# Performance work log

Measured on AMD Instinct MI355X. Metric: run time of the kernel, lower is better.

Reference implementation:

```python
import jax, jax.numpy as jnp
import numpy as np

B, F, S, K = 4, 1024, 2048, 7


def _activate_norm(x):
    # relu -> mean-center over last dim -> L2-normalize scaled by sqrt(n)
    out = jax.nn.relu(x)
    out = out - jnp.mean(out, axis=-1, keepdims=True)
    n = out.shape[-1]
    denom = (jnp.sqrt(jnp.sum(out * out, axis=-1, keepdims=True)) + 1e-5) * (n ** -0.5)
    return out / denom


def _causal_conv(x, w, k):
    # x: [B, C_in, S], w: [C_out, C_in, k]; left-pad by k-1 for causality
    return jax.lax.conv_general_dilated(
        x, w, window_strides=(1,), padding=[(k - 1, 0)],
        dimension_numbers=('NCH', 'OIH', 'NCH'))


def _feed_forward(x, w0, w1, k):
    return _causal_conv(_activate_norm(_causal_conv(x, w0, k)), w1, k)


def setup_inputs() -> dict:
    key = jax.random.key(0)
    ks = jax.random.split(key, 8)
    scale = 0.02
    inp = jax.random.normal(ks[0], (B, F, S), dtype=jnp.float32)
    pos_embd = jax.random.normal(ks[1], (1, F, S), dtype=jnp.float32) * scale
    divisor = jnp.arange(1, F + 1, dtype=jnp.float32).reshape(1, F, 1)
    ws = [jax.random.normal(ks[2 + i], (F, F, K), dtype=jnp.float32) * scale
          for i in range(6)]
    return {
        'inp': inp, 'pos_embd': pos_embd, 'divisor': divisor,
        'depth_w0': ws[0], 'depth_w1': ws[1],
        'point_w0': ws[2], 'point_w1': ws[3],
        'shift_w0': ws[4], 'shift_w1': ws[5],
    }


def reference(inp, pos_embd, divisor, depth_w0, depth_w1, point_w0, point_w1, shift_w0, shift_w1):
    out = inp + pos_embd
    depth = _feed_forward(out, depth_w0, depth_w1, K)
    point = _feed_forward(out, point_w0, point_w1, K)
    shift = _feed_forward(out, shift_w0, shift_w1, K)
    # linear attention: cumsum over feature axis (dim 1), matching depth.cumsum(1)
    return _activate_norm(inp * (jnp.cumsum(depth, axis=1) / divisor + point) + shift)
```

## Files before the change

### kernel.cpp

```cpp
#include <hip/hip_runtime.h>
#include <hip/hip_bf16.h>
#include <stdint.h>

#define B_ 4
#define F_ 1024
#define S_ 2048
#define K_ 7
#define SP_ (S_ + K_ - 1)
#define FC_ 64
#define NC_ (F_ / FC_)
#define FF_ ((size_t)F_ * F_)
#define BFS_ ((size_t)B_ * F_ * S_)
#define BSPF_ ((size_t)B_ * SP_ * F_)

using f32x4 = __attribute__((ext_vector_type(4))) float;
using s16x8 = __attribute__((ext_vector_type(8))) short;
using bf16 = __hip_bfloat16;

typedef const __attribute__((address_space(1))) void gvoid_t;
typedef __attribute__((address_space(3))) void lvoid_t;
__device__ __forceinline__ void async16(const void* g, void* l) {
    __builtin_amdgcn_global_load_lds((gvoid_t*)g, (lvoid_t*)l, 16, 0, 0);
}

__device__ __forceinline__ float bf2f(unsigned short u) {
    union { unsigned int i; float f; } c; c.i = ((unsigned int)u) << 16; return c.f;
}

#define FENCE() asm volatile("" ::: "memory")
#define BARRIER() do { FENCE(); __builtin_amdgcn_s_barrier(); FENCE(); } while (0)

__global__ void zero_pads(bf16* xT, bf16* hT, int nh) {
    int i = blockIdx.x * 256 + threadIdx.x;
    const int per = B_ * (K_ - 1) * F_;
    int total = (1 + nh) * per;
    if (i >= total) return;
    int r = i / per, o = i % per;
    int b = o / ((K_ - 1) * F_);
    int rr = o % ((K_ - 1) * F_);
    bf16 z = __float2bfloat16(0.0f);
    if (r == 0) xT[(size_t)b * SP_ * F_ + rr] = z;
    else        hT[(size_t)(r - 1) * BSPF_ + (size_t)b * SP_ * F_ + rr] = z;
}

__global__ void prep_x(const float* __restrict__ inp, const float* __restrict__ pos,
                       bf16* __restrict__ xT) {
    __shared__ bf16 tile[64][66];
    int b = blockIdx.z;
    int f0 = blockIdx.y * 64, s0 = blockIdx.x * 64;
    int tj = threadIdx.x & 63;
    int t4 = threadIdx.x >> 6;
#pragma unroll
    for (int r = 0; r < 16; ++r) {
        int i = r * 4 + t4;
        size_t off = (size_t)(f0 + i) * S_ + s0 + tj;
        float v = inp[(size_t)b * F_ * S_ + off] + pos[off];
        tile[i][tj] = __float2bfloat16(v);
    }
    __syncthreads();
#pragma unroll
    for (int r = 0; r < 16; ++r) {
        int j = r * 4 + t4;
        xT[(size_t)b * SP_ * F_ + (size_t)(6 + s0 + j) * F_ + f0 + tj] = tile[tj][j];
    }
}

__global__ void wconv(const float* __restrict__ w, bf16* __restrict__ wt) {
    int i = blockIdx.x * 256 + threadIdx.x;
    if (i >= F_ * F_) return;
    const float* src = w + (size_t)i * K_;
#pragma unroll
    for (int t = 0; t < K_; ++t)
        wt[(size_t)t * FF_ + i] = __float2bfloat16(src[t]);
}

#define MFMA_QUAD(MB, NB)                                                        \
    __builtin_amdgcn_s_setprio(1);                                               \
    _Pragma("unroll")                                                            \
    for (int kk = 0; kk < 2; ++kk) {                                             \
        _Pragma("unroll")                                                        \
        for (int m = 0; m < 4; ++m) {                                            \
            _Pragma("unroll")                                                    \
            for (int n = 0; n < 2; ++n) {                                        \
                acc[(MB) + m][(NB) + n] = __builtin_amdgcn_mfma_f32_16x16x32_bf16( \
                    af[m][kk], bfr[(NB) + n][kk], acc[(MB) + m][(NB) + n], 0, 0, 0); \
            }                                                                    \
        }                                                                        \
    }                                                                            \
    __builtin_amdgcn_s_setprio(0)

template <bool SPLIT>
__global__ __launch_bounds__(512, 2)
void conv_gemm8(const bf16* __restrict__ Wbase, const bf16* __restrict__ Xbase,
                bf16* __restrict__ O0, bf16* __restrict__ O1,
                long wStride, long xStride, long oStride) {
    __shared__ __align__(16) char lds[147456];

    int wg = blockIdx.x;
    int nchunk = gridDim.x >> 3;
    int swz = (wg & 7) * nchunk + (wg >> 3);
    int kp, r;
    if (SPLIT) { kp = swz & 1; r = swz >> 1; } else { kp = 0; r = swz; }
    int nt = r & 7;
    int mt = (r >> 3) & 3;
    int z  = r >> 5;
    int j = z >> 2, b = z & 3;
    const int kb0 = kp * 8;
    const int kbN = SPLIT ? 8 : 16;
    const int NTp = kbN * 7;

    const bf16* Wbr = Wbase + (size_t)j * wStride;
    const bf16* Xbr = Xbase + (size_t)j * xStride + (size_t)b * SP_ * F_;
    bf16* out = (kp ? O1 : O0) + (size_t)j * oStride + (size_t)b * F_ * S_;
    const int m0 = mt * 256, n0 = nt * 256;

    const int tid = threadIdx.x;
    const int lane = tid & 63, wid = tid >> 6;
    const int wm = wid >> 2, wn = wid & 3;

    const int tid16 = tid * 16;
    const int p0 = tid16, p1 = 8192 + tid16;
    const int lp0 = p0 ^ (((p0 >> 9) & 1) << 5);
    const int lp1 = p1 ^ (((p1 >> 9) & 1) << 5);
    const int stgO0 = (((lp0 >> 11) << 4) + ((lp0 >> 6) & 15)) * F_
                    + (((lp0 >> 10) & 1) << 5) + ((lp0 & 63) >> 1);
    const int stgO1 = (((lp1 >> 11) << 4) + ((lp1 >> 6) & 15)) * F_
                    + (((lp1 >> 10) & 1) << 5) + ((lp1 & 63) >> 1);
    const int bsrc = (((tid16 >> 11) << 4) + ((lp0 >> 6) & 15)) * F_
                   + (((lp0 >> 10) & 1) << 5) + ((lp0 & 63) >> 1);

    const int rA = lane & 15, cA = (lane >> 4) * 8;
    const int swzRC = (rA << 6) + ((cA << 1) ^ (((rA >> 3) & 1) << 5));
    const int aOffBase = wm * 16384 + swzRC;
    int addrB[7];
#pragma unroll
    for (int t = 0; t < 7; ++t) {
        int R = wn * 64 + rA + t;
        addrB[t] = ((R >> 4) << 11) + ((R & 15) << 6)
                 + ((cA << 1) ^ (((R >> 3) & 1) << 5));
    }

    f32x4 acc[8][4] = {};
    s16x8 af[4][2], bfr[4][2];

    auto STGA = [&](int regionByte, const bf16* src) {
        async16(src + stgO0, lds + regionByte + tid16);
        async16(src + stgO1, lds + regionByte + 8192 + tid16);
    };
    auto STGB = [&](int kb1, int pc) {
        const bf16* src = Xbr + (size_t)n0 * F_ + kb1 * 64 + bsrc + pc * 64 * F_;
        async16(src, lds + 65536 + (kb1 & 1) * 40960 + pc * 8192 + tid16);
    };
    auto ASRC = [&](int kb, int t, int h) {
        return Wbr + (size_t)t * FF_ + (size_t)(m0 + h * 128) * F_ + kb * 64;
    };

    STGB(kb0, 0); STGB(kb0, 1); STGB(kb0, 2); STGB(kb0, 3); STGB(kb0, 4);
    STGA(0,     ASRC(kb0, 0, 0));
    STGA(16384, ASRC(kb0, 0, 1));
    STGA(32768, ASRC(kb0, 1, 0));
    asm volatile("s_waitcnt vmcnt(2)" ::: "memory");
    BARRIER();

    for (int kb = kb0; kb < kb0 + kbN; ++kb) {
        const int bB = 65536 + (kb & 1) * 40960;
#pragma unroll
        for (int t = 0; t < 7; ++t) {
            const int ktl = (kb - kb0) * 7 + t;
            const int pA = (kb + t) & 1;
            const char* la = lds + pA * 32768 + aOffBase;
            const char* lb = lds + bB + addrB[t];
            const int t1 = (t == 6) ? 0 : t + 1;
            const int kb1 = (t == 6) ? kb + 1 : kb;
            const int t2 = (t >= 5) ? t - 5 : t + 2;
            const int kb2 = (t >= 5) ? kb + 1 : kb;
            const bool bstage = (t >= 1 && t <= 5) && (kb - kb0) < kbN - 1;

#pragma unroll
            for (int m = 0; m < 4; ++m) {
                af[m][0] = *(const s16x8*)(la + m * 2048);
                af[m][1] = *(const s16x8*)(la + m * 2048 + 1024);
            }
#pragma unroll
            for (int n = 0; n < 2; ++n) {
                bfr[n][0] = *(const s16x8*)(lb + n * 2048);
                bfr[n][1] = *(const s16x8*)(lb + n * 2048 + 1024);
            }
            if (ktl + 1 < NTp) STGA((pA ^ 1) * 32768 + 16384, ASRC(kb1, t1, 1));
            BARRIER();
            MFMA_QUAD(0, 0);
            BARRIER();

#pragma unroll
            for (int n = 0; n < 2; ++n) {
                bfr[2 + n][0] = *(const s16x8*)(lb + (2 + n) * 2048);
                bfr[2 + n][1] = *(const s16x8*)(lb + (2 + n) * 2048 + 1024);
            }
            if (bstage) STGB(kb + 1, t - 1);
            BARRIER();
            MFMA_QUAD(0, 2);
            BARRIER();

#pragma unroll
            for (int m = 0; m < 4; ++m) {
                af[m][0] = *(const s16x8*)(la + (4 + m) * 2048);
                af[m][1] = *(const s16x8*)(la + (4 + m) * 2048 + 1024);
            }
            BARRIER();
            MFMA_QUAD(4, 0);
            BARRIER();

            if (ktl + 2 < NTp) STGA(pA * 32768, ASRC(kb2, t2, 0));
            MFMA_QUAD(4, 2);
            if (ktl < NTp - 2) {
                if (bstage) { asm volatile("s_waitcnt vmcnt(3)" ::: "memory"); }
                else        { asm volatile("s_waitcnt vmcnt(2)" ::: "memory"); }
            } else {
                asm volatile("s_waitcnt vmcnt(0)" ::: "memory");
            }
            BARRIER();
        }
    }

    const int cm = (lane >> 4) * 4, cn = lane & 15;
#pragma unroll
    for (int mf = 0; mf < 8; ++mf)
#pragma unroll
        for (int nf = 0; nf < 4; ++nf)
#pragma unroll
            for (int r2 = 0; r2 < 4; ++r2) {
                int rr = m0 + wm * 128 + mf * 16 + cm + r2;
                int cc = n0 + wn * 64 + nf * 16 + cn;
                out[(size_t)rr * S_ + cc] = __float2bfloat16(acc[mf][nf][r2]);
            }
}

__global__ void addb(const bf16* __restrict__ a, bf16* __restrict__ d, long n8) {
    long i = (long)blockIdx.x * 256 + threadIdx.x;
    if (i >= n8) return;
    s16x8 va = ((const s16x8*)a)[i];
    s16x8 vd = ((const s16x8*)d)[i];
    s16x8 o;
#pragma unroll
    for (int e = 0; e < 8; ++e) {
        float f = bf2f((unsigned short)va[e]) + bf2f((unsigned short)vd[e]);
        o[e] = (short)__bfloat16_as_ushort(__float2bfloat16(f));
    }
    ((s16x8*)d)[i] = o;
}

__global__ void conv_gemm_small(const bf16* __restrict__ W7, const bf16* __restrict__ xT,
                                bf16* __restrict__ out) {
    __shared__ bf16 tA[128][64];
    __shared__ bf16 tB[128][64];
    int wg = blockIdx.x;
    int cpx = gridDim.x >> 3;
    int swz = (wg & 7) * cpx + (wg >> 3);
    int sx = swz & 15;
    int t1 = swz >> 4;
    int sy = t1 & 7;
    int b = t1 >> 3;
    const bf16* Xbr = xT + (size_t)b * SP_ * F_;
    bf16* ob = out + (size_t)b * F_ * S_;
    int m0 = sy * 128, n0 = sx * 128;
    int tid = threadIdx.x;
    int lane = tid & 63, wid = tid >> 6;
    int wm = wid >> 1, wn = wid & 1;
    f32x4 acc[4][4] = {};
    int srow = tid >> 3, cpart = tid & 7;
    for (int t = 0; t < K_; ++t) {
        const bf16* Wt = W7 + (size_t)t * FF_ + (size_t)m0 * F_;
        const bf16* Xt = Xbr + (size_t)(n0 + t) * F_;
        for (int kb = 0; kb < F_ / 64; ++kb) {
            const bf16* wa = Wt + kb * 64 + cpart * 8;
            const bf16* xa = Xt + kb * 64 + cpart * 8;
#pragma unroll
            for (int q = 0; q < 4; ++q) async16(wa + (size_t)(q * 32 + srow) * F_, &tA[q * 32 + srow][cpart * 8]);
#pragma unroll
            for (int q = 0; q < 4; ++q) async16(xa + (size_t)(q * 32 + srow) * F_, &tB[q * 32 + srow][cpart * 8]);
            __syncthreads();
#pragma unroll
            for (int kk = 0; kk < 2; ++kk) {
                int krow = kk * 32 + (lane >> 4) * 8;
                s16x8 a2[4], b2[4];
#pragma unroll
                for (int m = 0; m < 4; ++m) a2[m] = *(const s16x8*)&tA[wm * 64 + m * 16 + (lane & 15)][krow];
#pragma unroll
                for (int n = 0; n < 4; ++n) b2[n] = *(const s16x8*)&tB[wn * 64 + n * 16 + (lane & 15)][krow];
#pragma unroll
                for (int m = 0; m < 4; ++m)
#pragma unroll
                    for (int n = 0; n < 4; ++n)
                        acc[m][n] = __builtin_amdgcn_mfma_f32_16x16x32_bf16(a2[m], b2[n], acc[m][n], 0, 0, 0);
            }
            __syncthreads();
        }
    }
    int cm = (lane >> 4) * 4, cn = lane & 15;
#pragma unroll
    for (int m = 0; m < 4; ++m)
#pragma unroll
        for (int n = 0; n < 4; ++n)
#pragma unroll
            for (int r = 0; r < 4; ++r)
                ob[(size_t)(m0 + wm * 64 + m * 16 + cm + r) * S_ + n0 + wn * 64 + n * 16 + cn] =
                    __float2bfloat16(acc[m][n][r]);
}

__global__ void rowstats_bf16(const bf16* __restrict__ x, float2* __restrict__ stats) {
    int row = blockIdx.x * 4 + (threadIdx.x >> 6);
    int lane = threadIdx.x & 63;
    const bf16* p = x + (size_t)row * S_;
    float s1 = 0.f, s2 = 0.f;
#pragma unroll
    for (int q = 0; q < S_ / 512; ++q) {
        s16x8 v = *(const s16x8*)(p + q * 512 + lane * 8);
#pragma unroll
        for (int e = 0; e < 8; ++e) {
            float f = fmaxf(bf2f((unsigned short)v[e]), 0.f);
            s1 += f; s2 += f * f;
        }
    }
#pragma unroll
    for (int d = 32; d; d >>= 1) { s1 += __shfl_xor(s1, d); s2 += __shfl_xor(s2, d); }
    if (lane == 0) {
        float m = s1 / (float)S_;
        float ss = fmaxf(s2 - (float)S_ * m * m, 0.f);
        float denom = (sqrtf(ss) + 1e-5f) * (1.0f / sqrtf((float)S_));
        stats[row] = make_float2(m, 1.0f / denom);
    }
}

__global__ void rowstats_f32(const float* __restrict__ x, float2* __restrict__ stats) {
    int row = blockIdx.x * 4 + (threadIdx.x >> 6);
    int lane = threadIdx.x & 63;
    const float* p = x + (size_t)row * S_;
    float s1 = 0.f, s2 = 0.f;
#pragma unroll
    for (int q = 0; q < S_; q += 256) {
        float4 v = *(const float4*)(p + q + lane * 4);
        float a = fmaxf(v.x, 0.f), bb = fmaxf(v.y, 0.f);
        float c = fmaxf(v.z, 0.f), d = fmaxf(v.w, 0.f);
        s1 += a + bb + c + d;
        s2 += a * a + bb * bb + c * c + d * d;
    }
#pragma unroll
    for (int d = 32; d; d >>= 1) { s1 += __shfl_xor(s1, d); s2 += __shfl_xor(s2, d); }
    if (lane == 0) {
        float m = s1 / (float)S_;
        float ss = fmaxf(s2 - (float)S_ * m * m, 0.f);
        float denom = (sqrtf(ss) + 1e-5f) * (1.0f / sqrtf((float)S_));
        stats[row] = make_float2(m, 1.0f / denom);
    }
}

__global__ void normT(const bf16* __restrict__ x, const float2* __restrict__ stats,
                      bf16* __restrict__ hT) {
    __shared__ bf16 tile[64][72];
    int z = blockIdx.z;
    int f0 = blockIdx.y * 64, s0 = blockIdx.x * 64;
    const bf16* xb = x + (size_t)z * F_ * S_;
    bf16* hb = hT + (size_t)z * SP_ * F_;
    const float2* st = stats + (size_t)z * F_;
    int i = threadIdx.x >> 3;
    int c8 = threadIdx.x & 7;
#pragma unroll
    for (int p = 0; p < 2; ++p) {
        int r = i + p * 32;
        float2 s = st[f0 + r];
        s16x8 v = *(const s16x8*)(xb + (size_t)(f0 + r) * S_ + s0 + c8 * 8);
#pragma unroll
        for (int e = 0; e < 8; ++e) {
            float f = fmaxf(bf2f((unsigned short)v[e]), 0.f);
            tile[r][c8 * 8 + e] = __float2bfloat16((f - s.x) * s.y);
        }
    }
    __syncthreads();
    int tj = threadIdx.x & 63;
    int t4 = threadIdx.x >> 6;
#pragma unroll
    for (int r = 0; r < 16; ++r) {
        int jrow = r * 4 + t4;
        hb[(size_t)(6 + s0 + jrow) * F_ + f0 + tj] = tile[tj][jrow];
    }
}

__global__ void combine_partial(const bf16* __restrict__ depth,
                                float* __restrict__ partials) {
    int idx = blockIdx.x * 256 + threadIdx.x;
    int s = idx & (S_ - 1);
    int t = idx / S_;
    int fc = t % NC_;
    int b = t / NC_;
    const bf16* p = depth + (size_t)b * F_ * S_ + (size_t)(fc * FC_) * S_ + s;
    float acc = 0.f;
#pragma unroll
    for (int f = 0; f < FC_; ++f) acc += __bfloat162float(p[(size_t)f * S_]);
    partials[idx] = acc;
}

__global__ void combine_apply(const float* __restrict__ inp, const float* __restrict__ divisor,
                              const bf16* __restrict__ depth, const bf16* __restrict__ point,
                              const bf16* __restrict__ shiftb,
                              const float* __restrict__ partials, float* __restrict__ y) {
    int idx = blockIdx.x * 256 + threadIdx.x;
    int s = idx & (S_ - 1);
    int t = idx / S_;
    int fc = t % NC_;
    int b = t / NC_;
    float acc = 0.f;
    const float* pp = partials + (size_t)b * NC_ * S_ + s;
    for (int c = 0; c < fc; ++c) acc += pp[(size_t)c * S_];
    size_t base = (size_t)b * F_ * S_ + (size_t)(fc * FC_) * S_ + s;
#pragma unroll 4
    for (int f = 0; f < FC_; ++f) {
        size_t o = base + (size_t)f * S_;
        acc += __bfloat162float(depth[o]);
        float yv = inp[o] * (acc / divisor[fc * FC_ + f] + __bfloat162float(point[o]))
                 + __bfloat162float(shiftb[o]);
        y[o] = yv;
    }
}

__global__ void finalnorm(const float* __restrict__ y, const float2* __restrict__ stats,
                          float* __restrict__ out) {
    size_t i = (size_t)blockIdx.x * 256 + threadIdx.x;
    if (i >= (size_t)B_ * F_ * S_) return;
    float2 st = stats[i / S_];
    float v = fmaxf(y[i], 0.f);
    out[i] = (v - st.x) * st.y;
}

extern "C" void kernel_launch(void* const* d_in, const int* in_sizes, int n_in,
                              void* d_out, int out_size, void* d_ws, size_t ws_size,
                              hipStream_t stream) {
    const float* inp = (const float*)d_in[0];
    const float* pos = (const float*)d_in[1];
    const float* divisor = (const float*)d_in[2];
    const float* w[6] = { (const float*)d_in[3], (const float*)d_in[4],
                          (const float*)d_in[5], (const float*)d_in[6],
                          (const float*)d_in[7], (const float*)d_in[8] };
    float* out = (float*)d_out;

    size_t off = 0;
    auto alloc = [&](size_t bytes) {
        off = (off + 255) & ~(size_t)255;
        void* r = (char*)d_ws + off;
        off += bytes;
        return r;
    };

    const size_t needB = ((BSPF_ * 2 + 255) & ~255UL)
                       + ((3 * BSPF_ * 2 + 255) & ~255UL)
                       + ((3 * 7 * FF_ * 2 + 255) & ~255UL)
                       + ((3 * BFS_ * 2 + 255) & ~255UL)
                       + ((3 * BFS_ * 2 + 255) & ~255UL)
                       + ((3 * B_ * F_ * 8 + 255) & ~255UL)
                       + ((B_ * NC_ * S_ * 4 + 255) & ~255UL)
                       + 4096;
    const size_t needC = needB + ((3 * BFS_ * 2 + 255) & ~255UL);

    if (ws_size >= needB) {
        const bool splitK = (ws_size >= needC);
        bf16* xT   = (bf16*)alloc(BSPF_ * 2);
        bf16* hT3  = (bf16*)alloc(3 * BSPF_ * 2);
        bf16* Wb3  = (bf16*)alloc(3 * 7 * FF_ * 2);
        bf16* O3   = (bf16*)alloc(3 * BFS_ * 2);
        bf16* br3  = (bf16*)alloc(3 * BFS_ * 2);
        float2* stats3 = (float2*)alloc(3 * B_ * F_ * 8);
        float* partials = (float*)alloc(B_ * NC_ * S_ * 4);
        bf16* P0 = splitK ? (bf16*)alloc(3 * BFS_ * 2) : nullptr;
        float* ybuf = (float*)O3;
        const long n8 = (long)(3 * BFS_ / 8);

        zero_pads<<<(4 * B_ * (K_ - 1) * F_ + 255) / 256, 256, 0, stream>>>(xT, hT3, 3);
        prep_x<<<dim3(S_ / 64, F_ / 64, B_), 256, 0, stream>>>(inp, pos, xT);

        for (int j = 0; j < 3; ++j)
            wconv<<<F_ * F_ / 256, 256, 0, stream>>>(w[2 * j], Wb3 + j * 7 * FF_);
        if (splitK) {
            conv_gemm8<true><<<768, 512, 0, stream>>>(Wb3, xT, P0, O3, 7 * FF_, 0, BFS_);
            addb<<<(int)(n8 / 256), 256, 0, stream>>>(P0, O3, n8);
        } else {
            conv_gemm8<false><<<384, 512, 0, stream>>>(Wb3, xT, O3, O3, 7 * FF_, 0, BFS_);
        }
        rowstats_bf16<<<3 * B_ * F_ / 4, 256, 0, stream>>>(O3, stats3);
        normT<<<dim3(S_ / 64, F_ / 64, 12), 256, 0, stream>>>(O3, stats3, hT3);

        for (int j = 0; j < 3; ++j)
            wconv<<<F_ * F_ / 256, 256, 0, stream>>>(w[2 * j + 1], Wb3 + j * 7 * FF_);
        if (splitK) {
            conv_gemm8<true><<<768, 512, 0, stream>>>(Wb3, hT3, P0, br3, 7 * FF_, BSPF_, BFS_);
            addb<<<(int)(n8 / 256), 256, 0, stream>>>(P0, br3, n8);
        } else {
            conv_gemm8<false><<<384, 512, 0, stream>>>(Wb3, hT3, br3, br3, 7 * FF_, BSPF_, BFS_);
        }

        combine_partial<<<B_ * NC_ * S_ / 256, 256, 0, stream>>>(br3, partials);
        combine_apply<<<B_ * NC_ * S_ / 256, 256, 0, stream>>>(
            inp, divisor, br3, br3 + BFS_, br3 + 2 * BFS_, partials, ybuf);
        rowstats_f32<<<B_ * F_ / 4, 256, 0, stream>>>(ybuf, stats3);
        finalnorm<<<(B_ * F_ * S_) / 256, 256, 0, stream>>>(ybuf, stats3, out);
    } else {
        bf16* xT   = (bf16*)alloc(BSPF_ * 2);
        bf16* hT1  = (bf16*)alloc(BSPF_ * 2);
        bf16* Wb1  = (bf16*)alloc(7 * FF_ * 2);
        bf16* O1   = (bf16*)alloc(BFS_ * 2);
        bf16* br3  = (bf16*)alloc(3 * BFS_ * 2);
        float2* stats3 = (float2*)alloc(B_ * F_ * 8);
        float* partials = (float*)alloc(B_ * NC_ * S_ * 4);
        float* ybuf = (float*)xT;

        zero_pads<<<(2 * B_ * (K_ - 1) * F_ + 255) / 256, 256, 0, stream>>>(xT, hT1, 1);
        prep_x<<<dim3(S_ / 64, F_ / 64, B_), 256, 0, stream>>>(inp, pos, xT);

        for (int j = 0; j < 3; ++j) {
            wconv<<<F_ * F_ / 256, 256, 0, stream>>>(w[2 * j], Wb1);
            conv_gemm_small<<<16 * 8 * 4, 256, 0, stream>>>(Wb1, xT, O1);
            rowstats_bf16<<<B_ * F_ / 4, 256, 0, stream>>>(O1, stats3);
            normT<<<dim3(S_ / 64, F_ / 64, 4), 256, 0, stream>>>(O1, stats3, hT1);
            wconv<<<F_ * F_ / 256, 256, 0, stream>>>(w[2 * j + 1], Wb1);
            conv_gemm_small<<<16 * 8 * 4, 256, 0, stream>>>(Wb1, hT1, br3 + j * BFS_);
        }
        combine_partial<<<B_ * NC_ * S_ / 256, 256, 0, stream>>>(br3, partials);
        combine_apply<<<B_ * NC_ * S_ / 256, 256, 0, stream>>>(
            inp, divisor, br3, br3 + BFS_, br3 + 2 * BFS_, partials, ybuf);
        rowstats_f32<<<B_ * F_ / 4, 256, 0, stream>>>(ybuf, stats3);
        finalnorm<<<(B_ * F_ * S_) / 256, 256, 0, stream>>>(ybuf, stats3, out);
    }
}
```

Before: 737.3 us.

## Fuse split-K reductions into row-stats and combine kernels, store y in bf16

```diff
diff --git a/kernel.cpp b/kernel.cpp
--- a/kernel.cpp
+++ b/kernel.cpp
@@ -72,6 +72,18 @@
 #pragma unroll
     for (int t = 0; t < K_; ++t)
         wt[(size_t)t * FF_ + i] = __float2bfloat16(src[t]);
+}
+
+__global__ void wconv3(const float* __restrict__ w0, const float* __restrict__ w1,
+                       const float* __restrict__ w2, bf16* __restrict__ wt) {
+    int i = blockIdx.x * 256 + threadIdx.x;
+    int z = blockIdx.y;
+    const float* w = (z == 0) ? w0 : (z == 1 ? w1 : w2);
+    bf16* dst = wt + (size_t)z * 7 * FF_;
+    const float* src = w + (size_t)i * K_;
+#pragma unroll
+    for (int t = 0; t < K_; ++t)
+        dst[(size_t)t * FF_ + i] = __float2bfloat16(src[t]);
 }
 
 #define MFMA_QUAD(MB, NB)                                                        \
@@ -235,18 +247,36 @@
             }
 }
 
-__global__ void addb(const bf16* __restrict__ a, bf16* __restrict__ d, long n8) {
-    long i = (long)blockIdx.x * 256 + threadIdx.x;
-    if (i >= n8) return;
-    s16x8 va = ((const s16x8*)a)[i];
-    s16x8 vd = ((const s16x8*)d)[i];
-    s16x8 o;
-#pragma unroll
-    for (int e = 0; e < 8; ++e) {
-        float f = bf2f((unsigned short)va[e]) + bf2f((unsigned short)vd[e]);
-        o[e] = (short)__bfloat16_as_ushort(__float2bfloat16(f));
-    }
-    ((s16x8*)d)[i] = o;
+__global__ void addb_stats(const bf16* __restrict__ a, bf16* __restrict__ d,
+                           float2* __restrict__ stats) {
+    int row = blockIdx.x * 4 + (threadIdx.x >> 6);
+    int lane = threadIdx.x & 63;
+    const s16x8* pa = (const s16x8*)(a + (size_t)row * S_);
+    s16x8* pd = (s16x8*)(d + (size_t)row * S_);
+    float s1 = 0.f, s2 = 0.f;
+#pragma unroll
+    for (int q = 0; q < S_ / 512; ++q) {
+        s16x8 va = pa[q * 64 + lane];
+        s16x8 vd = pd[q * 64 + lane];
+        s16x8 o;
+#pragma unroll
+        for (int e = 0; e < 8; ++e) {
+            float f = bf2f((unsigned short)va[e]) + bf2f((unsigned short)vd[e]);
+            bf16 h = __float2bfloat16(f);
+            o[e] = (short)__bfloat16_as_ushort(h);
+            float rr = fmaxf(__bfloat162float(h), 0.f);
+            s1 += rr; s2 += rr * rr;
+        }
+        pd[q * 64 + lane] = o;
+    }
+#pragma unroll
+    for (int dd = 32; dd; dd >>= 1) { s1 += __shfl_xor(s1, dd); s2 += __shfl_xor(s2, dd); }
+    if (lane == 0) {
+        float m = s1 / (float)S_;
+        float ss = fmaxf(s2 - (float)S_ * m * m, 0.f);
+        float denom = (sqrtf(ss) + 1e-5f) * (1.0f / sqrtf((float)S_));
+        stats[row] = make_float2(m, 1.0f / denom);
+    }
 }
 
 __global__ void conv_gemm_small(const bf16* __restrict__ W7, const bf16* __restrict__ xT,
@@ -399,6 +429,23 @@
     partials[idx] = acc;
 }
 
+__global__ void combine_partial2(const bf16* __restrict__ dA, const bf16* __restrict__ dB,
+                                 float* __restrict__ partials) {
+    int idx = blockIdx.x * 256 + threadIdx.x;
+    int s = idx & (S_ - 1);
+    int t = idx / S_;
+    int fc = t % NC_;
+    int b = t / NC_;
+    size_t base = (size_t)b * F_ * S_ + (size_t)(fc * FC_) * S_ + s;
+    float acc = 0.f;
+#pragma unroll
+    for (int f = 0; f < FC_; ++f) {
+        size_t o = base + (size_t)f * S_;
+        acc += __bfloat162float(dA[o]) + __bfloat162float(dB[o]);
+    }
+    partials[idx] = acc;
+}
+
 __global__ void combine_apply(const float* __restrict__ inp, const float* __restrict__ divisor,
                               const bf16* __restrict__ depth, const bf16* __restrict__ point,
                               const bf16* __restrict__ shiftb,
@@ -422,6 +469,30 @@
     }
 }
 
+__global__ void combine_apply2(const float* __restrict__ inp, const float* __restrict__ divisor,
+                               const bf16* __restrict__ h0, const bf16* __restrict__ h1,
+                               const float* __restrict__ partials, bf16* __restrict__ y) {
+    int idx = blockIdx.x * 256 + threadIdx.x;
+    int s = idx & (S_ - 1);
+    int t = idx / S_;
+    int fc = t % NC_;
+    int b = t / NC_;
+    float acc = 0.f;
+    const float* pp = partials + (size_t)b * NC_ * S_ + s;
+    for (int c = 0; c < fc; ++c) acc += pp[(size_t)c * S_];
+    size_t base = (size_t)b * F_ * S_ + (size_t)(fc * FC_) * S_ + s;
+#pragma unroll 4
+    for (int f = 0; f < FC_; ++f) {
+        size_t o = base + (size_t)f * S_;
+        float dep = __bfloat162float(h0[o]) + __bfloat162float(h1[o]);
+        float poi = __bfloat162float(h0[o + BFS_]) + __bfloat162float(h1[o + BFS_]);
+        float shi = __bfloat162float(h0[o + 2 * BFS_]) + __bfloat162float(h1[o + 2 * BFS_]);
+        acc += dep;
+        float yv = inp[o] * (acc / divisor[fc * FC_ + f] + poi) + shi;
+        y[o] = __float2bfloat16(yv);
+    }
+}
+
 __global__ void finalnorm(const float* __restrict__ y, const float2* __restrict__ stats,
                           float* __restrict__ out) {
     size_t i = (size_t)blockIdx.x * 256 + threadIdx.x;
@@ -429,6 +500,20 @@
     float2 st = stats[i / S_];
     float v = fmaxf(y[i], 0.f);
     out[i] = (v - st.x) * st.y;
+}
+
+__global__ void finalnorm_bf(const bf16* __restrict__ y, const float2* __restrict__ stats,
+                             float* __restrict__ out) {
+    size_t i8 = (size_t)blockIdx.x * 256 + threadIdx.x;
+    size_t row = i8 >> 8;
+    float2 st = stats[row];
+    s16x8 v = ((const s16x8*)y)[i8];
+    float* o = out + i8 * 8;
+#pragma unroll
+    for (int e = 0; e < 8; ++e) {
+        float f = fmaxf(bf2f((unsigned short)v[e]), 0.f);
+        o[e] = (f - st.x) * st.y;
+    }
 }
 
 extern "C" void kernel_launch(void* const* d_in, const int* in_sizes, int n_in,
@@ -470,37 +555,38 @@
         float2* stats3 = (float2*)alloc(3 * B_ * F_ * 8);
         float* partials = (float*)alloc(B_ * NC_ * S_ * 4);
         bf16* P0 = splitK ? (bf16*)alloc(3 * BFS_ * 2) : nullptr;
-        float* ybuf = (float*)O3;
-        const long n8 = (long)(3 * BFS_ / 8);
 
         zero_pads<<<(4 * B_ * (K_ - 1) * F_ + 255) / 256, 256, 0, stream>>>(xT, hT3, 3);
         prep_x<<<dim3(S_ / 64, F_ / 64, B_), 256, 0, stream>>>(inp, pos, xT);
 
-        for (int j = 0; j < 3; ++j)
-            wconv<<<F_ * F_ / 256, 256, 0, stream>>>(w[2 * j], Wb3 + j * 7 * FF_);
+        wconv3<<<dim3(F_ * F_ / 256, 3), 256, 0, stream>>>(w[0], w[2], w[4], Wb3);
         if (splitK) {
             conv_gemm8<true><<<768, 512, 0, stream>>>(Wb3, xT, P0, O3, 7 * FF_, 0, BFS_);
-            addb<<<(int)(n8 / 256), 256, 0, stream>>>(P0, O3, n8);
+            addb_stats<<<3 * B_ * F_ / 4, 256, 0, stream>>>(P0, O3, stats3);
         } else {
             conv_gemm8<false><<<384, 512, 0, stream>>>(Wb3, xT, O3, O3, 7 * FF_, 0, BFS_);
-        }
-        rowstats_bf16<<<3 * B_ * F_ / 4, 256, 0, stream>>>(O3, stats3);
+            rowstats_bf16<<<3 * B_ * F_ / 4, 256, 0, stream>>>(O3, stats3);
+        }
         normT<<<dim3(S_ / 64, F_ / 64, 12), 256, 0, stream>>>(O3, stats3, hT3);
 
-        for (int j = 0; j < 3; ++j)
-            wconv<<<F_ * F_ / 256, 256, 0, stream>>>(w[2 * j + 1], Wb3 + j * 7 * FF_);
+        wconv3<<<dim3(F_ * F_ / 256, 3), 256, 0, stream>>>(w[1], w[3], w[5], Wb3);
         if (splitK) {
             conv_gemm8<true><<<768, 512, 0, stream>>>(Wb3, hT3, P0, br3, 7 * FF_, BSPF_, BFS_);
-            addb<<<(int)(n8 / 256), 256, 0, stream>>>(P0, br3, n8);
+            bf16* ybf = O3;
+            combine_partial2<<<B_ * NC_ * S_ / 256, 256, 0, stream>>>(P0, br3, partials);
+            combine_apply2<<<B_ * NC_ * S_ / 256, 256, 0, stream>>>(
+                inp, divisor, P0, br3, partials, ybf);
+            rowstats_bf16<<<B_ * F_ / 4, 256, 0, stream>>>(ybf, stats3);
+            finalnorm_bf<<<(int)(BFS_ / 8 / 256), 256, 0, stream>>>(ybf, stats3, out);
         } else {
             conv_gemm8<false><<<384, 512, 0, stream>>>(Wb3, hT3, br3, br3, 7 * FF_, BSPF_, BFS_);
-        }
-
-        combine_partial<<<B_ * NC_ * S_ / 256, 256, 0, stream>>>(br3, partials);
-        combine_apply<<<B_ * NC_ * S_ / 256, 256, 0, stream>>>(
-            inp, divisor, br3, br3 + BFS_, br3 + 2 * BFS_, partials, ybuf);
-        rowstats_f32<<<B_ * F_ / 4, 256, 0, stream>>>(ybuf, stats3);
-        finalnorm<<<(B_ * F_ * S_) / 256, 256, 0, stream>>>(ybuf, stats3, out);
+            float* ybuf = (float*)O3;
+            combine_partial<<<B_ * NC_ * S_ / 256, 256, 0, stream>>>(br3, partials);
+            combine_apply<<<B_ * NC_ * S_ / 256, 256, 0, stream>>>(
+                inp, divisor, br3, br3 + BFS_, br3 + 2 * BFS_, partials, ybuf);
+            rowstats_f32<<<B_ * F_ / 4, 256, 0, stream>>>(ybuf, stats3);
+            finalnorm<<<(B_ * F_ * S_) / 256, 256, 0, stream>>>(ybuf, stats3, out);
+        }
     } else {
         bf16* xT   = (bf16*)alloc(BSPF_ * 2);
         bf16* hT1  = (bf16*)alloc(BSPF_ * 2);
```

Result: faster. 682.3 us (-7.5%).
